# Performance work log

Hardware: AMD Instinct MI355X
Metric: run time of the kernel (lower is better)

The kernel has to match this reference:

```python
import jax, jax.numpy as jnp
import numpy as np

N_NODES = 100000
N_EDGES = 1600000
D_IN = 64
D_OUT = 64


def setup_inputs() -> dict:
    key = jax.random.key(0)
    k1, k2, k3, k4, k5, k6 = jax.random.split(key, 6)
    feat = jax.random.normal(k1, (N_NODES, D_IN), dtype=jnp.float32)
    src = jax.random.randint(k2, (N_EDGES,), 0, N_NODES, dtype=jnp.int64)
    dst = jax.random.randint(k3, (N_EDGES,), 0, N_NODES, dtype=jnp.int64)
    edge_weight = jax.random.uniform(k4, (N_EDGES,), dtype=jnp.float32)
    # Xavier-uniform with relu gain, as in reset_parameters
    gain = float(np.sqrt(2.0))
    bound = gain * float(np.sqrt(6.0 / (D_IN + D_OUT)))
    W_neigh = jax.random.uniform(k5, (D_OUT, D_IN), dtype=jnp.float32, minval=-bound, maxval=bound)
    W_self = jax.random.uniform(k6, (D_OUT, D_IN), dtype=jnp.float32, minval=-bound, maxval=bound)
    bias = jnp.zeros((D_OUT,), dtype=jnp.float32)
    return {"feat": feat, "src": src, "dst": dst, "edge_weight": edge_weight,
            "W_neigh": W_neigh, "W_self": W_self, "bias": bias}


def reference(feat, src, dst, edge_weight, W_neigh, W_self, bias):
    n = feat.shape[0]
    # feat_drop with p=0.0 is identity; in_feats == out_feats so lin_before_mp is False
    # message: u_mul_e -> gather src features, scale by edge weight  [E, D_IN]
    m = feat[src] * edge_weight[:, None]
    # mean reduce over incoming edges (zero for isolated dst nodes, matching DGL)
    s = jax.ops.segment_sum(m, dst, num_segments=n)
    deg = jax.ops.segment_sum(jnp.ones_like(edge_weight), dst, num_segments=n)
    neigh = s / jnp.maximum(deg, 1.0)[:, None]
    h_neigh = neigh @ W_neigh.T
    h_self = feat @ W_self.T
    return h_self + h_neigh + bias
```

## Files before the change

kernel.cpp:

```cpp
#include <hip/hip_runtime.h>
#include <hip/hip_fp16.h>

constexpr int N_NODES = 100000;
constexpr int N_EDGES = 1600000;
constexpr int D = 64;

constexpr int BSH    = 5;
constexpr int BN     = 1 << BSH;
constexpr int NBUCK  = N_NODES / BN;
constexpr int NN2    = N_NODES;
constexpr int NCNTB  = 800;
constexpr int EPB2   = N_EDGES / NCNTB;
constexpr int NCVT   = (N_NODES * D / 4) / 256;
constexpr int BINSH  = 9;
constexpr int BINSZ  = 1 << BINSH;
constexpr int NBINS  = (NN2 + BINSZ - 1) >> BINSH;
constexpr int CHUNK  = 2048;
constexpr int NPA    = (N_EDGES + CHUNK - 1) / CHUNK;

constexpr size_t OFF_NSTART   = 400384;
constexpr size_t OFF_BINCNT   = 800768;
constexpr size_t OFF_BINSTART = 801280;
constexpr size_t OFF_BINCUR   = 802304;
constexpr size_t OFF_W16      = 1602048;
constexpr size_t OFF_FEAT16   = 1634816;
constexpr size_t OFF_ENT2     = OFF_FEAT16 + (size_t)N_NODES * D * 2;
constexpr size_t OFF_ENTA     = OFF_ENT2 + (size_t)N_EDGES * 8;
constexpr size_t WS_NEEDED    = OFF_ENTA + (size_t)N_EDGES * 8;

typedef short  bf16x8 __attribute__((ext_vector_type(8)));
typedef float  f32x4  __attribute__((ext_vector_type(4)));

__device__ __forceinline__ unsigned short f2bf(float f) {
    unsigned u = __float_as_uint(f);
    u += 0x7fffu + ((u >> 16) & 1u);
    return (unsigned short)(u >> 16);
}

__device__ __forceinline__ float h2f_lo(unsigned u) {
    return __half2float(__ushort_as_half((unsigned short)(u & 0xFFFFu)));
}
__device__ __forceinline__ float h2f_hi(unsigned u) {
    return __half2float(__ushort_as_half((unsigned short)(u >> 16)));
}

__device__ __forceinline__ void split8(float4 p0, float4 p1, bf16x8& hi, bf16x8& lo) {
    float f[8] = {p0.x, p0.y, p0.z, p0.w, p1.x, p1.y, p1.z, p1.w};
#pragma unroll
    for (int i = 0; i < 8; ++i) {
        const unsigned short h = f2bf(f[i]);
        const float hf = __uint_as_float((unsigned)h << 16);
        hi[i] = (short)h;
        lo[i] = (short)f2bf(f[i] - hf);
    }
}

__global__ __launch_bounds__(256) void k_zero(int* __restrict__ bincnt) {
    int i = blockIdx.x * 256 + threadIdx.x;
    if (i < NBINS) bincnt[i] = 0;
}

__global__ __launch_bounds__(256) void k_pre(const float4* __restrict__ feat4,
                                             unsigned short* __restrict__ feat16,
                                             const float* __restrict__ Wn,
                                             const float* __restrict__ Ws,
                                             unsigned short* __restrict__ W16,
                                             const int* __restrict__ dst,
                                             int* __restrict__ bincnt) {
    __shared__ int l[NBINS];
    const int b   = blockIdx.x;
    const int tid = threadIdx.x;
    if (b < NCVT) {
        const int i = b * 256 + tid;
        float4 v = feat4[i];
        ushort4 o;
        o.x = __half_as_ushort(__float2half_rn(v.x));
        o.y = __half_as_ushort(__float2half_rn(v.y));
        o.z = __half_as_ushort(__float2half_rn(v.z));
        o.w = __half_as_ushort(__float2half_rn(v.w));
        *(ushort4*)&feat16[(size_t)i * 4] = o;
    } else if (b < NCVT + NCNTB) {
        for (int i = tid; i < NBINS; i += 256) l[i] = 0;
        __syncthreads();
        const int base = (b - NCVT) * EPB2;
        for (int k = tid; k < EPB2; k += 256)
            atomicAdd(&l[dst[base + k] >> BINSH], 1);
        __syncthreads();
        for (int i = tid; i < NBINS; i += 256)
            if (l[i]) atomicAdd(&bincnt[i], l[i]);
    } else {
        for (int e = tid; e < D * 128; e += 256) {
            const int j = e >> 7, k = e & 127;
            const float w = (k < D) ? Ws[j * D + k] : Wn[j * D + (k - D)];
            const unsigned short h = f2bf(w);
            const float hf = __uint_as_float((unsigned)h << 16);
            W16[e] = h;
            W16[D * 128 + e] = f2bf(w - hf);
        }
    }
}

__global__ __launch_bounds__(256) void k_scan_bins(const int* __restrict__ bincnt,
                                                   int* __restrict__ binstart,
                                                   int* __restrict__ bincur) {
    __shared__ int s[256];
    const int t = threadIdx.x;
    const int v = (t < NBINS) ? bincnt[t] : 0;
    s[t] = v;
    __syncthreads();
    for (int off = 1; off < 256; off <<= 1) {
        int u = (t >= off) ? s[t - off] : 0;
        __syncthreads();
        s[t] += u;
        __syncthreads();
    }
    if (t < NBINS) { binstart[t] = s[t] - v; bincur[t] = s[t] - v; }
    if (t == 0) binstart[NBINS] = N_EDGES;
}

__global__ __launch_bounds__(256) void k_place_a(const int* __restrict__ src,
                                                 const int* __restrict__ dst,
                                                 const float* __restrict__ ew,
                                                 int* __restrict__ bincur,
                                                 uint2* __restrict__ entriesA) {
    __shared__ __align__(16) uint2 stage[CHUNK];
    __shared__ unsigned char sbin[CHUNK];
    __shared__ int hist[NBINS], lstart[NBINS], lcur[NBINS], gbase[NBINS];
    __shared__ int s[256];
    const int tid = threadIdx.x;
    const int e0  = blockIdx.x * CHUNK;
    const int cnt = min(CHUNK, N_EDGES - e0);

    for (int i = tid; i < NBINS; i += 256) hist[i] = 0;
    __syncthreads();
    for (int k = tid; k < cnt; k += 256)
        atomicAdd(&hist[dst[e0 + k] >> BINSH], 1);
    __syncthreads();
    {
        const int v = (tid < NBINS) ? hist[tid] : 0;
        s[tid] = v;
        __syncthreads();
        for (int off = 1; off < 256; off <<= 1) {
            int u = (tid >= off) ? s[tid - off] : 0;
            __syncthreads();
            s[tid] += u;
            __syncthreads();
        }
        if (tid < NBINS) {
            const int ex = s[tid] - v;
            lstart[tid] = ex;
            lcur[tid]   = ex;
            gbase[tid]  = v ? atomicAdd(&bincur[tid], v) : 0;
        }
    }
    __syncthreads();
    for (int k = tid; k < cnt; k += 256) {
        const int d = dst[e0 + k];
        const int b = d >> BINSH;
        const int p = atomicAdd(&lcur[b], 1);
        stage[p] = make_uint2((unsigned)src[e0 + k] | ((unsigned)(d & (BINSZ - 1)) << 17),
                              __float_as_uint(ew[e0 + k]));
        sbin[p]  = (unsigned char)b;
    }
    __syncthreads();
    for (int j = tid; j < cnt; j += 256) {
        const int b = sbin[j];
        entriesA[gbase[b] + (j - lstart[b])] = stage[j];
    }
}

__global__ __launch_bounds__(1024) void k_sortbin(const int* __restrict__ binstart,
                                                  const uint2* __restrict__ entriesA,
                                                  int* __restrict__ nstart,
                                                  uint2* __restrict__ entries2) {
    __shared__ int h[BINSZ];
    __shared__ int sc[BINSZ];
    __shared__ int cur[BINSZ];
    const int tid = threadIdx.x;
    const int b   = blockIdx.x;
    const int s0  = binstart[b];
    const int cnt = binstart[b + 1] - s0;

    if (tid < BINSZ) h[tid] = 0;
    __syncthreads();
    for (int k = tid; k < cnt; k += 1024)
        atomicAdd(&h[entriesA[s0 + k].x >> 17], 1);
    __syncthreads();
    const int v = (tid < BINSZ) ? h[tid] : 0;
    if (tid < BINSZ) sc[tid] = v;
    __syncthreads();
    for (int off = 1; off < BINSZ; off <<= 1) {
        int u = 0;
        if (tid < BINSZ && tid >= off) u = sc[tid - off];
        __syncthreads();
        if (tid < BINSZ) sc[tid] += u;
        __syncthreads();
    }
    if (tid < BINSZ) {
        const int pos = s0 + sc[tid] - v;
        cur[tid] = pos;
        const int n = (b << BINSH) + tid;
        if (n < NN2) nstart[n] = pos;
    }
    if (b == NBINS - 1 && tid == 0) nstart[NN2] = N_EDGES;
    __syncthreads();
    for (int k = tid; k < cnt; k += 1024) {
        const uint2 a = entriesA[s0 + k];
        const int p = atomicAdd(&cur[a.x >> 17], 1);
        entries2[p] = make_uint2(a.x & 0x1FFFFu, a.y);
    }
}

__global__ __launch_bounds__(256, 8) void k_bucket(
    const uint2* __restrict__ feat16u2,
    const float* __restrict__ feat32,
    const int* __restrict__ nstart,
    const uint2* __restrict__ entries2,
    const unsigned short* __restrict__ W16,
    const float* __restrict__ bias,
    float* __restrict__ out) {
    __shared__ __align__(16) float aggrow[BN * 68];
    __shared__ int hh[BN], st[BN];
    const int tid = threadIdx.x;
    const int b   = blockIdx.x;

    if (tid < BN) {
        const int s = nstart[b * BN + tid];
        const int e = nstart[b * BN + tid + 1];
        st[tid] = s;
        hh[tid] = e - s;
    }
    __syncthreads();

    const int wave = tid >> 6, lane = tid & 63;
    const int group = lane >> 4, gl = lane & 15;
    for (int t = 0; t < 8; ++t) {
        const int dl  = wave * 8 + t;
        const int ss  = st[dl];
        const int deg = hh[dl];
        const int se  = ss + deg;
        float4 acc = make_float4(0.f, 0.f, 0.f, 0.f);
        int e = ss + group;
        for (; e + 4 < se; e += 8) {
            const uint2 en0 = entries2[e];
            const uint2 en1 = entries2[e + 4];
            const uint2 p0  = feat16u2[(size_t)en0.x * 16 + gl];
            const uint2 p1  = feat16u2[(size_t)en1.x * 16 + gl];
            const float w0  = __uint_as_float(en0.y);
            const float w1  = __uint_as_float(en1.y);
            acc.x = fmaf(h2f_lo(p0.x), w0, acc.x);
            acc.y = fmaf(h2f_hi(p0.x), w0, acc.y);
            acc.z = fmaf(h2f_lo(p0.y), w0, acc.z);
            acc.w = fmaf(h2f_hi(p0.y), w0, acc.w);
            acc.x = fmaf(h2f_lo(p1.x), w1, acc.x);
            acc.y = fmaf(h2f_hi(p1.x), w1, acc.y);
            acc.z = fmaf(h2f_lo(p1.y), w1, acc.z);
            acc.w = fmaf(h2f_hi(p1.y), w1, acc.w);
        }
        if (e < se) {
            const uint2 en = entries2[e];
            const float w  = __uint_as_float(en.y);
            const uint2 p  = feat16u2[(size_t)en.x * 16 + gl];
            acc.x = fmaf(h2f_lo(p.x), w, acc.x);
            acc.y = fmaf(h2f_hi(p.x), w, acc.y);
            acc.z = fmaf(h2f_lo(p.y), w, acc.z);
            acc.w = fmaf(h2f_hi(p.y), w, acc.w);
        }
#pragma unroll
        for (int m = 16; m <= 32; m <<= 1) {
            acc.x += __shfl_xor(acc.x, m);
            acc.y += __shfl_xor(acc.y, m);
            acc.z += __shfl_xor(acc.z, m);
            acc.w += __shfl_xor(acc.w, m);
        }
        if (group == 0) {
            const float inv = 1.0f / fmaxf((float)deg, 1.0f);
            float4 o = make_float4(acc.x * inv, acc.y * inv, acc.z * inv, acc.w * inv);
            *(float4*)&aggrow[dl * 68 + gl * 4] = o;
        }
    }
    __syncthreads();

    const int quad = lane >> 4, r = lane & 15;
    const int rowh = wave & 1, colh = wave >> 1;
    const int node0 = b * BN + rowh * 16;
    int arow = node0 + r;
    if (arow > N_NODES - 1) arow = N_NODES - 1;

    bf16x8 ahi[4], alo[4];
    {
        const float* fp = &feat32[(size_t)arow * 64 + quad * 8];
        split8(*(const float4*)fp,        *(const float4*)(fp + 4),  ahi[0], alo[0]);
        split8(*(const float4*)(fp + 32), *(const float4*)(fp + 36), ahi[1], alo[1]);
        const float* ap = &aggrow[(rowh * 16 + r) * 68 + quad * 8];
        split8(*(const float4*)ap,        *(const float4*)(ap + 4),  ahi[2], alo[2]);
        split8(*(const float4*)(ap + 32), *(const float4*)(ap + 36), ahi[3], alo[3]);
    }

    const unsigned short* W16lo = W16 + D * 128;
    f32x4 acc4[2] = {};
#pragma unroll
    for (int nti = 0; nti < 2; ++nti) {
        const int nt = colh * 2 + nti;
#pragma unroll
        for (int kc = 0; kc < 4; ++kc) {
            const size_t wo = (size_t)(nt * 16 + r) * 128 + kc * 32 + quad * 8;
            const bf16x8 bhi = *(const bf16x8*)&W16[wo];
            const bf16x8 blo = *(const bf16x8*)&W16lo[wo];
            acc4[nti] = __builtin_amdgcn_mfma_f32_16x16x32_bf16(ahi[kc], bhi, acc4[nti], 0, 0, 0);
            acc4[nti] = __builtin_amdgcn_mfma_f32_16x16x32_bf16(alo[kc], bhi, acc4[nti], 0, 0, 0);
            acc4[nti] = __builtin_amdgcn_mfma_f32_16x16x32_bf16(ahi[kc], blo, acc4[nti], 0, 0, 0);
        }
    }

#pragma unroll
    for (int nti = 0; nti < 2; ++nti) {
        const int nt = colh * 2 + nti;
        const float bv = bias[nt * 16 + r];
#pragma unroll
        for (int reg = 0; reg < 4; ++reg) {
            const int m = node0 + quad * 4 + reg;
            if (m < N_NODES) out[(size_t)m * 64 + nt * 16 + r] = acc4[nti][reg] + bv;
        }
    }
}

__global__ __launch_bounds__(256) void fb_zero(float4* __restrict__ out4,
                                               float* __restrict__ deg) {
    const int stride = gridDim.x * blockDim.x;
    int i = blockIdx.x * blockDim.x + threadIdx.x;
    const int total4 = (N_NODES * D) / 4;
    for (int idx = i; idx < total4; idx += stride)
        out4[idx] = make_float4(0.f, 0.f, 0.f, 0.f);
    for (int idx = i; idx < N_NODES; idx += stride)
        deg[idx] = 0.f;
}

__global__ __launch_bounds__(256) void fb_scatter(
    const float* __restrict__ feat, const int* __restrict__ src,
    const int* __restrict__ dst, const float* __restrict__ ew,
    float* __restrict__ out, float* __restrict__ deg) {
    const int gid  = blockIdx.x * blockDim.x + threadIdx.x;
    const int e    = gid >> 6;
    const int lane = gid & 63;
    if (e >= N_EDGES) return;
    atomicAdd(&out[(size_t)dst[e] * D + lane], feat[(size_t)src[e] * D + lane] * ew[e]);
    if (lane == 0) atomicAdd(&deg[dst[e]], 1.0f);
}

__global__ __launch_bounds__(256) void fb_finalize(
    const float* __restrict__ feat, const float* __restrict__ Wn,
    const float* __restrict__ Ws, const float* __restrict__ bias,
    const float* __restrict__ deg, float* __restrict__ out) {
    __shared__ float lWn[D * 65];
    __shared__ float lWs[D * 65];
    for (int idx = threadIdx.x; idx < D * D; idx += 256) {
        const int r = idx >> 6, c = idx & 63;
        lWn[r * 65 + c] = Wn[idx];
        lWs[r * 65 + c] = Ws[idx];
    }
    __syncthreads();
    const int wave = threadIdx.x >> 6;
    const int lane = threadIdx.x & 63;
    const int n = blockIdx.x * 4 + wave;
    if (n >= N_NODES) return;
    const float f  = feat[(size_t)n * D + lane];
    const float sv = out[(size_t)n * D + lane];
    const float inv = 1.0f / fmaxf(deg[n], 1.0f);
    float acc_s = 0.f, acc_n = 0.f;
#pragma unroll
    for (int k = 0; k < D; ++k) {
        acc_s += __shfl(f, k)  * lWs[lane * 65 + k];
        acc_n += __shfl(sv, k) * lWn[lane * 65 + k];
    }
    out[(size_t)n * D + lane] = acc_s + acc_n * inv + bias[lane];
}

extern "C" void kernel_launch(void* const* d_in, const int* in_sizes, int n_in,
                              void* d_out, int out_size, void* d_ws, size_t ws_size,
                              hipStream_t stream) {
    const float* feat = (const float*)d_in[0];
    const int*   src  = (const int*)  d_in[1];
    const int*   dst  = (const int*)  d_in[2];
    const float* ew   = (const float*)d_in[3];
    const float* Wn   = (const float*)d_in[4];
    const float* Ws   = (const float*)d_in[5];
    const float* bias = (const float*)d_in[6];
    float* out = (float*)d_out;
    char* ws = (char*)d_ws;

    if (ws_size >= WS_NEEDED) {
        int* nstart   = (int*)(ws + OFF_NSTART);
        int* bincnt   = (int*)(ws + OFF_BINCNT);
        int* binstart = (int*)(ws + OFF_BINSTART);
        int* bincur   = (int*)(ws + OFF_BINCUR);
        unsigned short* W16    = (unsigned short*)(ws + OFF_W16);
        unsigned short* feat16 = (unsigned short*)(ws + OFF_FEAT16);
        uint2* entries2 = (uint2*)(ws + OFF_ENT2);
        uint2* entriesA = (uint2*)(ws + OFF_ENTA);

        k_zero     <<<1, 256, 0, stream>>>(bincnt);
        k_pre      <<<NCVT + NCNTB + 1, 256, 0, stream>>>((const float4*)feat, feat16,
                                                          Wn, Ws, W16, dst, bincnt);
        k_scan_bins<<<1, 256, 0, stream>>>(bincnt, binstart, bincur);
        k_place_a  <<<NPA, 256, 0, stream>>>(src, dst, ew, bincur, entriesA);
        k_sortbin  <<<NBINS, 1024, 0, stream>>>(binstart, entriesA, nstart, entries2);
        k_bucket   <<<NBUCK, 256, 0, stream>>>((const uint2*)feat16, feat, nstart,
                                               entries2, W16, bias, out);
    } else {
        float* deg = (float*)d_ws;
        fb_zero<<<2048, 256, 0, stream>>>((float4*)out, deg);
        fb_scatter<<<(N_EDGES * 64) / 256, 256, 0, stream>>>(feat, src, dst, ew, out, deg);
        fb_finalize<<<(N_NODES + 3) / 4, 256, 0, stream>>>(feat, Wn, Ws, bias, deg, out);
    }
}
```

Before: 240.4 us.

## Drop per-node sort; aggregate bin edges via LDS atomics in fused kernel

```diff
diff --git a/kernel.cpp b/kernel.cpp
--- a/kernel.cpp
+++ b/kernel.cpp
@@ -5,27 +5,23 @@
 constexpr int N_EDGES = 1600000;
 constexpr int D = 64;
 
-constexpr int BSH    = 5;
-constexpr int BN     = 1 << BSH;
-constexpr int NBUCK  = N_NODES / BN;
-constexpr int NN2    = N_NODES;
 constexpr int NCNTB  = 800;
 constexpr int EPB2   = N_EDGES / NCNTB;
 constexpr int NCVT   = (N_NODES * D / 4) / 256;
 constexpr int BINSH  = 9;
 constexpr int BINSZ  = 1 << BINSH;
-constexpr int NBINS  = (NN2 + BINSZ - 1) >> BINSH;
+constexpr int NBINS  = (N_NODES + BINSZ - 1) >> BINSH;
 constexpr int CHUNK  = 2048;
 constexpr int NPA    = (N_EDGES + CHUNK - 1) / CHUNK;
-
-constexpr size_t OFF_NSTART   = 400384;
-constexpr size_t OFF_BINCNT   = 800768;
-constexpr size_t OFF_BINSTART = 801280;
-constexpr size_t OFF_BINCUR   = 802304;
-constexpr size_t OFF_W16      = 1602048;
-constexpr size_t OFF_FEAT16   = 1634816;
-constexpr size_t OFF_ENT2     = OFF_FEAT16 + (size_t)N_NODES * D * 2;
-constexpr size_t OFF_ENTA     = OFF_ENT2 + (size_t)N_EDGES * 8;
+constexpr int SUBN   = 128;
+constexpr int NAGG   = NBINS * 4;
+
+constexpr size_t OFF_BINCNT   = 0;
+constexpr size_t OFF_BINSTART = 1024;
+constexpr size_t OFF_BINCUR   = 2048;
+constexpr size_t OFF_W16      = 4096;
+constexpr size_t OFF_FEAT16   = 36864;
+constexpr size_t OFF_ENTA     = OFF_FEAT16 + (size_t)N_NODES * D * 2;
 constexpr size_t WS_NEEDED    = OFF_ENTA + (size_t)N_EDGES * 8;
 
 typedef short  bf16x8 __attribute__((ext_vector_type(8)));
@@ -53,6 +49,10 @@
         hi[i] = (short)h;
         lo[i] = (short)f2bf(f[i] - hf);
     }
+}
+
+__device__ __forceinline__ float4 scale4(float4 v, float s) {
+    return make_float4(v.x * s, v.y * s, v.z * s, v.w * s);
 }
 
 __global__ __launch_bounds__(256) void k_zero(int* __restrict__ bincnt) {
@@ -169,158 +169,119 @@
     }
 }
 
-__global__ __launch_bounds__(1024) void k_sortbin(const int* __restrict__ binstart,
-                                                  const uint2* __restrict__ entriesA,
-                                                  int* __restrict__ nstart,
-                                                  uint2* __restrict__ entries2) {
-    __shared__ int h[BINSZ];
-    __shared__ int sc[BINSZ];
-    __shared__ int cur[BINSZ];
-    const int tid = threadIdx.x;
-    const int b   = blockIdx.x;
-    const int s0  = binstart[b];
-    const int cnt = binstart[b + 1] - s0;
-
-    if (tid < BINSZ) h[tid] = 0;
-    __syncthreads();
-    for (int k = tid; k < cnt; k += 1024)
-        atomicAdd(&h[entriesA[s0 + k].x >> 17], 1);
-    __syncthreads();
-    const int v = (tid < BINSZ) ? h[tid] : 0;
-    if (tid < BINSZ) sc[tid] = v;
-    __syncthreads();
-    for (int off = 1; off < BINSZ; off <<= 1) {
-        int u = 0;
-        if (tid < BINSZ && tid >= off) u = sc[tid - off];
-        __syncthreads();
-        if (tid < BINSZ) sc[tid] += u;
-        __syncthreads();
-    }
-    if (tid < BINSZ) {
-        const int pos = s0 + sc[tid] - v;
-        cur[tid] = pos;
-        const int n = (b << BINSH) + tid;
-        if (n < NN2) nstart[n] = pos;
-    }
-    if (b == NBINS - 1 && tid == 0) nstart[NN2] = N_EDGES;
-    __syncthreads();
-    for (int k = tid; k < cnt; k += 1024) {
-        const uint2 a = entriesA[s0 + k];
-        const int p = atomicAdd(&cur[a.x >> 17], 1);
-        entries2[p] = make_uint2(a.x & 0x1FFFFu, a.y);
-    }
-}
-
-__global__ __launch_bounds__(256, 8) void k_bucket(
+__global__ __launch_bounds__(256, 4) void k_agg(
     const uint2* __restrict__ feat16u2,
     const float* __restrict__ feat32,
-    const int* __restrict__ nstart,
-    const uint2* __restrict__ entries2,
+    const int* __restrict__ binstart,
+    const uint2* __restrict__ entriesA,
     const unsigned short* __restrict__ W16,
     const float* __restrict__ bias,
     float* __restrict__ out) {
-    __shared__ __align__(16) float aggrow[BN * 68];
-    __shared__ int hh[BN], st[BN];
-    const int tid = threadIdx.x;
-    const int b   = blockIdx.x;
-
-    if (tid < BN) {
-        const int s = nstart[b * BN + tid];
-        const int e = nstart[b * BN + tid + 1];
-        st[tid] = s;
-        hh[tid] = e - s;
+    __shared__ __align__(16) float aggrow[SUBN * 68];
+    __shared__ int deg[SUBN];
+    const int tid  = threadIdx.x;
+    const int b512 = blockIdx.x >> 2;
+    const unsigned q = blockIdx.x & 3;
+    const int s0   = binstart[b512];
+    const int cnt  = binstart[b512 + 1] - s0;
+
+    for (int i = tid; i < SUBN * 68 / 4; i += 256)
+        ((float4*)aggrow)[i] = make_float4(0.f, 0.f, 0.f, 0.f);
+    if (tid < SUBN) deg[tid] = 0;
+    __syncthreads();
+
+    const int g = tid >> 4, gl = tid & 15;
+    int i = g;
+    for (; i + 16 < cnt; i += 32) {
+        const uint2 a0 = entriesA[s0 + i];
+        const uint2 a1 = entriesA[s0 + i + 16];
+        const bool m0 = ((a0.x >> 24) & 3u) == q;
+        const bool m1 = ((a1.x >> 24) & 3u) == q;
+        uint2 p0, p1;
+        if (m0) p0 = feat16u2[(size_t)(a0.x & 0x1FFFFu) * 16 + gl];
+        if (m1) p1 = feat16u2[(size_t)(a1.x & 0x1FFFFu) * 16 + gl];
+        if (m0) {
+            const float w = __uint_as_float(a0.y);
+            float* r = &aggrow[(int)((a0.x >> 17) & 127u) * 68 + gl * 4];
+            atomicAdd(r + 0, h2f_lo(p0.x) * w);
+            atomicAdd(r + 1, h2f_hi(p0.x) * w);
+            atomicAdd(r + 2, h2f_lo(p0.y) * w);
+            atomicAdd(r + 3, h2f_hi(p0.y) * w);
+            if (gl == 0) atomicAdd(&deg[(a0.x >> 17) & 127u], 1);
+        }
+        if (m1) {
+            const float w = __uint_as_float(a1.y);
+            float* r = &aggrow[(int)((a1.x >> 17) & 127u) * 68 + gl * 4];
+            atomicAdd(r + 0, h2f_lo(p1.x) * w);
+            atomicAdd(r + 1, h2f_hi(p1.x) * w);
+            atomicAdd(r + 2, h2f_lo(p1.y) * w);
+            atomicAdd(r + 3, h2f_hi(p1.y) * w);
+            if (gl == 0) atomicAdd(&deg[(a1.x >> 17) & 127u], 1);
+        }
+    }
+    for (; i < cnt; i += 16) {
+        const uint2 a = entriesA[s0 + i];
+        if (((a.x >> 24) & 3u) == q) {
+            const uint2 p = feat16u2[(size_t)(a.x & 0x1FFFFu) * 16 + gl];
+            const float w = __uint_as_float(a.y);
+            float* r = &aggrow[(int)((a.x >> 17) & 127u) * 68 + gl * 4];
+            atomicAdd(r + 0, h2f_lo(p.x) * w);
+            atomicAdd(r + 1, h2f_hi(p.x) * w);
+            atomicAdd(r + 2, h2f_lo(p.y) * w);
+            atomicAdd(r + 3, h2f_hi(p.y) * w);
+            if (gl == 0) atomicAdd(&deg[(a.x >> 17) & 127u], 1);
+        }
     }
     __syncthreads();
 
     const int wave = tid >> 6, lane = tid & 63;
-    const int group = lane >> 4, gl = lane & 15;
-    for (int t = 0; t < 8; ++t) {
-        const int dl  = wave * 8 + t;
-        const int ss  = st[dl];
-        const int deg = hh[dl];
-        const int se  = ss + deg;
-        float4 acc = make_float4(0.f, 0.f, 0.f, 0.f);
-        int e = ss + group;
-        for (; e + 4 < se; e += 8) {
-            const uint2 en0 = entries2[e];
-            const uint2 en1 = entries2[e + 4];
-            const uint2 p0  = feat16u2[(size_t)en0.x * 16 + gl];
-            const uint2 p1  = feat16u2[(size_t)en1.x * 16 + gl];
-            const float w0  = __uint_as_float(en0.y);
-            const float w1  = __uint_as_float(en1.y);
-            acc.x = fmaf(h2f_lo(p0.x), w0, acc.x);
-            acc.y = fmaf(h2f_hi(p0.x), w0, acc.y);
-            acc.z = fmaf(h2f_lo(p0.y), w0, acc.z);
-            acc.w = fmaf(h2f_hi(p0.y), w0, acc.w);
-            acc.x = fmaf(h2f_lo(p1.x), w1, acc.x);
-            acc.y = fmaf(h2f_hi(p1.x), w1, acc.y);
-            acc.z = fmaf(h2f_lo(p1.y), w1, acc.z);
-            acc.w = fmaf(h2f_hi(p1.y), w1, acc.w);
-        }
-        if (e < se) {
-            const uint2 en = entries2[e];
-            const float w  = __uint_as_float(en.y);
-            const uint2 p  = feat16u2[(size_t)en.x * 16 + gl];
-            acc.x = fmaf(h2f_lo(p.x), w, acc.x);
-            acc.y = fmaf(h2f_hi(p.x), w, acc.y);
-            acc.z = fmaf(h2f_lo(p.y), w, acc.z);
-            acc.w = fmaf(h2f_hi(p.y), w, acc.w);
-        }
-#pragma unroll
-        for (int m = 16; m <= 32; m <<= 1) {
-            acc.x += __shfl_xor(acc.x, m);
-            acc.y += __shfl_xor(acc.y, m);
-            acc.z += __shfl_xor(acc.z, m);
-            acc.w += __shfl_xor(acc.w, m);
-        }
-        if (group == 0) {
-            const float inv = 1.0f / fmaxf((float)deg, 1.0f);
-            float4 o = make_float4(acc.x * inv, acc.y * inv, acc.z * inv, acc.w * inv);
-            *(float4*)&aggrow[dl * 68 + gl * 4] = o;
-        }
-    }
-    __syncthreads();
-
     const int quad = lane >> 4, r = lane & 15;
-    const int rowh = wave & 1, colh = wave >> 1;
-    const int node0 = b * BN + rowh * 16;
-    int arow = node0 + r;
-    if (arow > N_NODES - 1) arow = N_NODES - 1;
-
-    bf16x8 ahi[4], alo[4];
-    {
-        const float* fp = &feat32[(size_t)arow * 64 + quad * 8];
-        split8(*(const float4*)fp,        *(const float4*)(fp + 4),  ahi[0], alo[0]);
-        split8(*(const float4*)(fp + 32), *(const float4*)(fp + 36), ahi[1], alo[1]);
-        const float* ap = &aggrow[(rowh * 16 + r) * 68 + quad * 8];
-        split8(*(const float4*)ap,        *(const float4*)(ap + 4),  ahi[2], alo[2]);
-        split8(*(const float4*)(ap + 32), *(const float4*)(ap + 36), ahi[3], alo[3]);
-    }
-
+    const int nbase = b512 * 512 + (int)q * SUBN;
     const unsigned short* W16lo = W16 + D * 128;
-    f32x4 acc4[2] = {};
-#pragma unroll
-    for (int nti = 0; nti < 2; ++nti) {
-        const int nt = colh * 2 + nti;
-#pragma unroll
-        for (int kc = 0; kc < 4; ++kc) {
-            const size_t wo = (size_t)(nt * 16 + r) * 128 + kc * 32 + quad * 8;
-            const bf16x8 bhi = *(const bf16x8*)&W16[wo];
-            const bf16x8 blo = *(const bf16x8*)&W16lo[wo];
-            acc4[nti] = __builtin_amdgcn_mfma_f32_16x16x32_bf16(ahi[kc], bhi, acc4[nti], 0, 0, 0);
-            acc4[nti] = __builtin_amdgcn_mfma_f32_16x16x32_bf16(alo[kc], bhi, acc4[nti], 0, 0, 0);
-            acc4[nti] = __builtin_amdgcn_mfma_f32_16x16x32_bf16(ahi[kc], blo, acc4[nti], 0, 0, 0);
-        }
-    }
-
-#pragma unroll
-    for (int nti = 0; nti < 2; ++nti) {
-        const int nt = colh * 2 + nti;
-        const float bv = bias[nt * 16 + r];
-#pragma unroll
-        for (int reg = 0; reg < 4; ++reg) {
-            const int m = node0 + quad * 4 + reg;
-            if (m < N_NODES) out[(size_t)m * 64 + nt * 16 + r] = acc4[nti][reg] + bv;
+
+#pragma unroll
+    for (int rti = 0; rti < 2; ++rti) {
+        const int rt = wave * 2 + rti;
+        const int node0 = nbase + rt * 16;
+        int arow = node0 + r;
+        if (arow > N_NODES - 1) arow = N_NODES - 1;
+
+        bf16x8 ahi[4], alo[4];
+        {
+            const float* fp = &feat32[(size_t)arow * 64 + quad * 8];
+            split8(*(const float4*)fp,        *(const float4*)(fp + 4),  ahi[0], alo[0]);
+            split8(*(const float4*)(fp + 32), *(const float4*)(fp + 36), ahi[1], alo[1]);
+            const int lrow = rt * 16 + r;
+            const float inv = 1.0f / fmaxf((float)deg[lrow], 1.0f);
+            const float* ap = &aggrow[lrow * 68 + quad * 8];
+            split8(scale4(*(const float4*)ap,        inv),
+                   scale4(*(const float4*)(ap + 4),  inv), ahi[2], alo[2]);
+            split8(scale4(*(const float4*)(ap + 32), inv),
+                   scale4(*(const float4*)(ap + 36), inv), ahi[3], alo[3]);
+        }
+
+        f32x4 acc4[4] = {};
+#pragma unroll
+        for (int nt = 0; nt < 4; ++nt) {
+#pragma unroll
+            for (int kc = 0; kc < 4; ++kc) {
+                const size_t wo = (size_t)(nt * 16 + r) * 128 + kc * 32 + quad * 8;
+                const bf16x8 bhi = *(const bf16x8*)&W16[wo];
+                const bf16x8 blo = *(const bf16x8*)&W16lo[wo];
+                acc4[nt] = __builtin_amdgcn_mfma_f32_16x16x32_bf16(ahi[kc], bhi, acc4[nt], 0, 0, 0);
+                acc4[nt] = __builtin_amdgcn_mfma_f32_16x16x32_bf16(alo[kc], bhi, acc4[nt], 0, 0, 0);
+                acc4[nt] = __builtin_amdgcn_mfma_f32_16x16x32_bf16(ahi[kc], blo, acc4[nt], 0, 0, 0);
+            }
+        }
+
+#pragma unroll
+        for (int nt = 0; nt < 4; ++nt) {
+            const float bv = bias[nt * 16 + r];
+#pragma unroll
+            for (int reg = 0; reg < 4; ++reg) {
+                const int m = node0 + quad * 4 + reg;
+                if (m < N_NODES) out[(size_t)m * 64 + nt * 16 + r] = acc4[nt][reg] + bv;
+            }
         }
     }
 }
@@ -390,13 +351,11 @@
     char* ws = (char*)d_ws;
 
     if (ws_size >= WS_NEEDED) {
-        int* nstart   = (int*)(ws + OFF_NSTART);
         int* bincnt   = (int*)(ws + OFF_BINCNT);
         int* binstart = (int*)(ws + OFF_BINSTART);
         int* bincur   = (int*)(ws + OFF_BINCUR);
         unsigned short* W16    = (unsigned short*)(ws + OFF_W16);
         unsigned short* feat16 = (unsigned short*)(ws + OFF_FEAT16);
-        uint2* entries2 = (uint2*)(ws + OFF_ENT2);
         uint2* entriesA = (uint2*)(ws + OFF_ENTA);
 
         k_zero     <<<1, 256, 0, stream>>>(bincnt);
@@ -404,9 +363,8 @@
                                                           Wn, Ws, W16, dst, bincnt);
         k_scan_bins<<<1, 256, 0, stream>>>(bincnt, binstart, bincur);
         k_place_a  <<<NPA, 256, 0, stream>>>(src, dst, ew, bincur, entriesA);
-        k_sortbin  <<<NBINS, 1024, 0, stream>>>(binstart, entriesA, nstart, entries2);
-        k_bucket   <<<NBUCK, 256, 0, stream>>>((const uint2*)feat16, feat, nstart,
-                                               entries2, W16, bias, out);
+        k_agg      <<<NAGG, 256, 0, stream>>>((const uint2*)feat16, feat, binstart,
+                                              entriesA, W16, bias, out);
     } else {
         float* deg = (float*)d_ws;
         fb_zero<<<2048, 256, 0, stream>>>((float4*)out, deg);
```

Result: slower. 861.0 us (+258.1%).
